# Performance work log

Hardware: AMD Instinct MI355X
Metric: run time of the kernel (lower is better)

## Reference

```python
import jax, jax.numpy as jnp
import numpy as np
from math import sqrt

D_MODEL, D_COND, N_HEADS = 512, 768, 8
B, H, W, L_COND = 8, 64, 64, 256


def setup_inputs() -> dict:
    key = jax.random.key(0)
    ks = jax.random.split(key, 7)
    return {
        "image": jax.random.normal(ks[0], (B, D_MODEL, H, W), jnp.float32),
        "cond": jax.random.normal(ks[1], (B, L_COND, D_COND), jnp.float32),
        "attention_mask": jnp.zeros((B, H * W, L_COND), jnp.float32),
        "Wq": jax.random.normal(ks[2], (D_MODEL, D_MODEL), jnp.float32) * 0.02,
        "Wk": jax.random.normal(ks[3], (D_MODEL, D_COND), jnp.float32) * 0.02,
        "Wv": jax.random.normal(ks[4], (D_MODEL, D_COND), jnp.float32) * 0.02,
        "Wo": jax.random.normal(ks[5], (D_MODEL, D_MODEL), jnp.float32) * 0.02,
        "bo": jnp.zeros((D_MODEL,), jnp.float32),
    }


def reference(image, cond, attention_mask, Wq, Wk, Wv, Wo, bo):
    b, d, h, w = image.shape
    L = h * w
    n = N_HEADS
    dh = d // n
    scale = sqrt(dh)
    # b d h w -> b l d
    x = image.reshape(b, d, L).transpose(0, 2, 1)
    # projections (torch Linear: y = x @ W.T), split heads: b l (n dh) -> b n l dh
    q = (x @ Wq.T).reshape(b, L, n, dh).transpose(0, 2, 1, 3)
    k = (cond @ Wk.T).reshape(b, -1, n, dh).transpose(0, 2, 1, 3)
    v = (cond @ Wv.T).reshape(b, -1, n, dh).transpose(0, 2, 1, 3)
    attn = jnp.einsum("bnqd,bnkd->bnqk", q, k) / scale
    attn = attn + attention_mask[:, None]  # b 1 L L_cond
    p = jax.nn.softmax(attn, axis=-1)
    o = jnp.einsum("bnqk,bnkd->bnqd", p, v)  # b n L dh
    # b n (h w) dh -> b (n dh) h w
    o = o.transpose(0, 1, 3, 2).reshape(b, d, h, w)
    # 1x1 conv == per-pixel linear over channels
    out = jnp.einsum("oc,bchw->bohw", Wo, o) + bo[None, :, None, None]
    return out
```

## Files before the change

kernel.cpp:

```cpp
#include <hip/hip_runtime.h>

typedef __bf16 bf16x8 __attribute__((ext_vector_type(8)));
typedef float f32x4 __attribute__((ext_vector_type(4)));
typedef short s4 __attribute__((ext_vector_type(4)));
typedef unsigned short ush;

#define DEV __device__ __forceinline__


DEV ush f2bf(float x){
  union { float f; unsigned u; } v; v.f = x;
  unsigned r = v.u + 0x7FFFu + ((v.u >> 16) & 1u);
  return (ush)(r >> 16);
}

DEV short bfcast(float x){
  union { __bf16 h; short s; } cv; cv.h = (__bf16)x; return cv.s;
}

DEV void gload_lds16(const ush* g, ush* l){
  __builtin_amdgcn_global_load_lds(
      (const __attribute__((address_space(1))) unsigned int*)g,
      (__attribute__((address_space(3))) unsigned int*)l, 16, 0, 0);
}

__global__ __launch_bounds__(256) void tc_kernel(const float* __restrict__ img, ush* __restrict__ xT){
  __shared__ float tile[32][34];
  const int b = blockIdx.z;
  const int l0 = blockIdx.x << 5, c0 = blockIdx.y << 5;
  const int rj = threadIdx.x >> 3, cj = threadIdx.x & 7;
  const float* src = img + ((size_t)b*512 + c0 + rj)*4096 + l0 + (cj<<2);
  float4 v = *(const float4*)src;
  *(float2*)&tile[rj][(cj<<2)]     = make_float2(v.x, v.y);
  *(float2*)&tile[rj][(cj<<2) + 2] = make_float2(v.z, v.w);
  __syncthreads();
  s4 o;
  #pragma unroll
  for (int k = 0; k < 4; ++k) o[k] = bfcast(tile[(cj<<2) + k][rj]);
  *(s4*)(xT + ((size_t)b*4096 + l0 + rj)*512 + c0 + (cj<<2)) = o;
}

__global__ __launch_bounds__(256) void cvt_kernel(const float* c0,const float* c1,const float* c2,
                                                  const float* c3,const float* c4,
                                                  ush* o0, ush* o1, ush* o2, ush* o3, ush* o4){
  const int N0=1572864, N1=262144, N2=393216, N3=393216, N4=262144;
  const int stride = gridDim.x * blockDim.x;
  for (int i = blockIdx.x*blockDim.x + threadIdx.x; i < N0+N1+N2+N3+N4; i += stride){
    int j = i; const float* s; ush* d;
    if (j < N0){ s=c0; d=o0; }
    else { j-=N0; if (j<N1){s=c1;d=o1;}
      else { j-=N1; if (j<N2){s=c2;d=o2;}
        else { j-=N2; if (j<N3){s=c3;d=o3;} else { j-=N3; s=c4; d=o4; } } } }
    d[j] = f2bf(s[j]);
  }
}

DEV void gemm_core(const ush* __restrict__ Ag, long long a_row0, int lda,
                   const ush* __restrict__ Bg, long long b_row0, int ldb,
                   int K, ush* As, ush* Bs, f32x4 acc[4][4])
{
  const int t = threadIdx.x;
  const int lane = t & 63;
  const int wid = t >> 6, wr = wid >> 1, wc = wid & 1;
  #pragma unroll
  for (int mt=0;mt<4;mt++)
    #pragma unroll
    for (int nt=0;nt<4;nt++) acc[mt][nt] = f32x4{0.f,0.f,0.f,0.f};

  const int nk = K >> 6;
  for (int kt = 0; kt < nk; ++kt){
    const int k0 = kt << 6;
    #pragma unroll
    for (int r = 0; r < 4; ++r){
      int idx = (r<<8) + t;
      int row = idx >> 3, slot = idx & 7;
      gload_lds16(Ag + (a_row0 + row)*(long long)lda + k0 + ((slot ^ (row&7))<<3), As + idx*8);
    }
    #pragma unroll
    for (int r = 0; r < 4; ++r){
      int idx = (r<<8) + t;
      int row = idx >> 3, slot = idx & 7;
      gload_lds16(Bg + (b_row0 + row)*(long long)ldb + k0 + ((slot ^ (row&7))<<3), Bs + idx*8);
    }
    __syncthreads();
    #pragma unroll
    for (int kk = 0; kk < 2; ++kk){
      bf16x8 af[4], bfv[4];
      #pragma unroll
      for (int mt=0;mt<4;mt++){
        int row = (wr<<6) + (mt<<4) + (lane & 15);
        int byte = (row<<7) + (kk<<6) + ((lane>>4)<<4);
        byte ^= (row & 7) << 4;
        af[mt] = *(const bf16x8*)((const char*)As + byte);
      }
      #pragma unroll
      for (int nt=0;nt<4;nt++){
        int row = (wc<<6) + (nt<<4) + (lane & 15);
        int byte = (row<<7) + (kk<<6) + ((lane>>4)<<4);
        byte ^= (row & 7) << 4;
        bfv[nt] = *(const bf16x8*)((const char*)Bs + byte);
      }
      #pragma unroll
      for (int mt=0;mt<4;mt++)
        #pragma unroll
        for (int nt=0;nt<4;nt++)
          acc[mt][nt] = __builtin_amdgcn_mfma_f32_16x16x32_bf16(af[mt], bfv[nt], acc[mt][nt], 0,0,0);
    }
    __syncthreads();
  }
}

__global__ __launch_bounds__(256,2) void qproj_kernel(const ush* __restrict__ xT, const ush* __restrict__ Wqb,
                                                      ush* __restrict__ Qg){
  __shared__ ush As[8192], Bs[8192];
  f32x4 acc[4][4];
  const int mb = blockIdx.x & 255, nb = blockIdx.x >> 8;
  gemm_core(xT, (long long)mb*128, 512, Wqb, (long long)nb*128, 512, 512, As, Bs, acc);
  const int lane = threadIdx.x & 63, wid = threadIdx.x >> 6, wr = wid>>1, wc = wid&1;
  #pragma unroll
  for (int mt=0;mt<4;mt++)
    #pragma unroll
    for (int nt=0;nt<4;nt++)
      #pragma unroll
      for (int r=0;r<4;r++){
        int m = mb*128 + (wr<<6) + (mt<<4) + ((lane>>4)<<2) + r;
        int n = (nb<<7) + (wc<<6) + (nt<<4) + (lane&15);
        int bb = m >> 12, l = m & 4095, hh = n >> 6, dh = n & 63;
        Qg[(((size_t)(bb*8 + hh)*4096 + l)<<6) + dh] = f2bf(acc[mt][nt][r] * 0.180336880f);
      }
}

__global__ __launch_bounds__(256,2) void kvproj_kernel(const ush* __restrict__ cb, const ush* __restrict__ Wkb,
                                                       const ush* __restrict__ Wvb, ush* __restrict__ Kg,
                                                       ush* __restrict__ Vt){
  __shared__ ush As[8192], Bs[8192];
  f32x4 acc[4][4];
  const int which = blockIdx.z;
  const int nb = blockIdx.x & 3, mb = blockIdx.x >> 2;
  gemm_core(cb, (long long)mb*128, 768, which ? Wvb : Wkb, (long long)nb*128, 768, 768, As, Bs, acc);
  const int lane = threadIdx.x & 63, wid = threadIdx.x >> 6, wr = wid>>1, wc = wid&1;
  #pragma unroll
  for (int mt=0;mt<4;mt++)
    #pragma unroll
    for (int nt=0;nt<4;nt++)
      #pragma unroll
      for (int r=0;r<4;r++){
        int m = mb*128 + (wr<<6) + (mt<<4) + ((lane>>4)<<2) + r;
        int n = (nb<<7) + (wc<<6) + (nt<<4) + (lane&15);
        int bb = m >> 8, j = m & 255;
        ush val = f2bf(acc[mt][nt][r]);
        if (!which) Kg[(((size_t)(bb*256 + j))<<9) + n] = val;
        else { int hh = n>>6, dh = n&63; Vt[(((size_t)((bb*8+hh)*64 + dh))<<8) + j] = val; }
      }
}

__global__ __launch_bounds__(512,1) void attn_kernel(const ush* __restrict__ Qg, const ush* __restrict__ Kg,
                                                     const ush* __restrict__ Vg, const float* __restrict__ mask,
                                                     ush* __restrict__ Oc){
  extern __shared__ char smem[];
  ush* Ks = (ush*)smem;
  ush* Vs = (ush*)(smem + 32768);
  const int t = threadIdx.x, lane = t & 63, wid = t >> 6;
  const int qb = blockIdx.x, h = blockIdx.y, b = blockIdx.z;
  const float L2E = 1.44269504f;

  #pragma unroll
  for (int r = 0; r < 4; ++r){
    int idx = (r<<9) + t;
    int j = idx >> 3, slot = idx & 7;
    gload_lds16(Kg + ((size_t)(b*256 + j))*512 + h*64 + ((slot ^ (j&7))<<3), Ks + idx*8);
  }
  #pragma unroll
  for (int r = 0; r < 4; ++r){
    int idx = (r<<9) + t;
    int dh = idx >> 5, slot = idx & 31;
    gload_lds16(Vg + ((size_t)((b*8 + h)*64 + dh))*256 + ((((slot&7) ^ (dh&7)) | (slot&24))<<3), Vs + idx*8);
  }
  __syncthreads();

  const int l15 = lane & 15, kg = lane >> 4;
  const ush* Qbase = Qg + ((size_t)(b*8 + h)*4096)*64;
  const int q00 = qb*1024 + wid*128;

  #pragma unroll 1
  for (int mp = 0; mp < 4; ++mp){
    const int qA = q00 + mp*32 + l15;
    const int qB = qA + 16;
    bf16x8 qf00 = *(const bf16x8*)(Qbase + (size_t)qA*64 + (kg<<3));
    bf16x8 qf01 = *(const bf16x8*)(Qbase + (size_t)qA*64 + 32 + (kg<<3));
    bf16x8 qf10 = *(const bf16x8*)(Qbase + (size_t)qB*64 + (kg<<3));
    bf16x8 qf11 = *(const bf16x8*)(Qbase + (size_t)qB*64 + 32 + (kg<<3));
    const float* mrowA = mask + ((size_t)b*4096 + qA)*256 + (kg<<2);
    const float* mrowB = mrowA + (16<<8);

    f32x4 oaccA[4], oaccB[4];
    #pragma unroll
    for (int tl=0;tl<4;++tl){ oaccA[tl] = f32x4{0.f,0.f,0.f,0.f}; oaccB[tl] = f32x4{0.f,0.f,0.f,0.f}; }
    float mA = 0.f, mB = 0.f;
    f32x4 svA = f32x4{0.f,0.f,0.f,0.f}, svB = f32x4{0.f,0.f,0.f,0.f};

    #pragma unroll 1
    for (int qt = 0; qt < 4; ++qt){
      f32x4 sA[4], sB[4];
      #pragma unroll
      for (int nt=0;nt<4;++nt){ sA[nt] = f32x4{0.f,0.f,0.f,0.f}; sB[nt] = f32x4{0.f,0.f,0.f,0.f}; }
      #pragma unroll
      for (int nt=0;nt<4;++nt){
        int row = (qt<<6) + (nt<<4) + l15;
        const char* kb = (const char*)Ks + (row<<7);
        int sw = (row&7)<<4;
        bf16x8 kf0 = *(const bf16x8*)(kb + ((kg<<4) ^ sw));
        bf16x8 kf1 = *(const bf16x8*)(kb + (((kg<<4)+64) ^ sw));
        sA[nt] = __builtin_amdgcn_mfma_f32_16x16x32_bf16(kf0, qf00, sA[nt], 0,0,0);
        sA[nt] = __builtin_amdgcn_mfma_f32_16x16x32_bf16(kf1, qf01, sA[nt], 0,0,0);
        sB[nt] = __builtin_amdgcn_mfma_f32_16x16x32_bf16(kf0, qf10, sB[nt], 0,0,0);
        sB[nt] = __builtin_amdgcn_mfma_f32_16x16x32_bf16(kf1, qf11, sB[nt], 0,0,0);
      }

      float mxA = -3.0e38f, mxB = -3.0e38f;
      #pragma unroll
      for (int nt=0;nt<4;++nt){
        float4 va = *(const float4*)(mrowA + (qt<<6) + (nt<<4));
        float4 vb = *(const float4*)(mrowB + (qt<<6) + (nt<<4));
        sA[nt][0] = fmaf(va.x, L2E, sA[nt][0]); sA[nt][1] = fmaf(va.y, L2E, sA[nt][1]);
        sA[nt][2] = fmaf(va.z, L2E, sA[nt][2]); sA[nt][3] = fmaf(va.w, L2E, sA[nt][3]);
        sB[nt][0] = fmaf(vb.x, L2E, sB[nt][0]); sB[nt][1] = fmaf(vb.y, L2E, sB[nt][1]);
        sB[nt][2] = fmaf(vb.z, L2E, sB[nt][2]); sB[nt][3] = fmaf(vb.w, L2E, sB[nt][3]);
        #pragma unroll
        for (int r=0;r<4;++r){ mxA = fmaxf(mxA, sA[nt][r]); mxB = fmaxf(mxB, sB[nt][r]); }
      }
      mxA = fmaxf(mxA, __shfl_xor(mxA, 16, 64));
      mxA = fmaxf(mxA, __shfl_xor(mxA, 32, 64));
      mxB = fmaxf(mxB, __shfl_xor(mxB, 16, 64));
      mxB = fmaxf(mxB, __shfl_xor(mxB, 32, 64));

      if (qt == 0){
        mA = mxA; mB = mxB;
      } else if (!__all(fmaxf(mxA - mA, mxB - mB) <= 8.f)){
        float mnA = fmaxf(mA, mxA), mnB = fmaxf(mB, mxB);
        float aA = exp2f(mA - mnA), aB = exp2f(mB - mnB);
        #pragma unroll
        for (int r=0;r<4;++r){ svA[r] *= aA; svB[r] *= aB; }
        #pragma unroll
        for (int tl=0;tl<4;++tl)
          #pragma unroll
          for (int r=0;r<4;++r){ oaccA[tl][r] *= aA; oaccB[tl][r] *= aB; }
        mA = mnA; mB = mnB;
      }

      #pragma unroll
      for (int nt=0;nt<4;++nt){
        s4 pA, pB;
        #pragma unroll
        for (int r=0;r<4;++r){
          float pa = exp2f(sA[nt][r] - mA);
          float pb = exp2f(sB[nt][r] - mB);
          svA[r] += pa; svB[r] += pb;
          pA[r] = bfcast(pa); pB[r] = bfcast(pb);
        }
        #pragma unroll
        for (int tl=0;tl<4;++tl){
          int dr = (tl<<4) + l15;
          int off = ((qt<<7) + (nt<<5) + (kg<<3)) ^ ((dr&7)<<4);
          s4 vf = *(const s4*)((const char*)Vs + (dr<<9) + off);
          oaccA[tl] = __builtin_amdgcn_mfma_f32_16x16x16bf16_1k(vf, pA, oaccA[tl], 0,0,0);
          oaccB[tl] = __builtin_amdgcn_mfma_f32_16x16x16bf16_1k(vf, pB, oaccB[tl], 0,0,0);
        }
      }
      __builtin_amdgcn_sched_barrier(0);
    }

    float sAt = (svA[0]+svA[1]) + (svA[2]+svA[3]);
    float sBt = (svB[0]+svB[1]) + (svB[2]+svB[3]);
    sAt += __shfl_xor(sAt, 16, 64); sAt += __shfl_xor(sAt, 32, 64);
    sBt += __shfl_xor(sBt, 16, 64); sBt += __shfl_xor(sBt, 32, 64);
    const float rlA = 1.f / sAt, rlB = 1.f / sBt;
    #pragma unroll
    for (int tl=0;tl<4;++tl){
      s4 ovA, ovB;
      #pragma unroll
      for (int r=0;r<4;++r){ ovA[r] = bfcast(oaccA[tl][r] * rlA); ovB[r] = bfcast(oaccB[tl][r] * rlB); }
      *(s4*)(Oc + (((size_t)b*4096 + qA)<<9) + h*64 + (tl<<4) + (kg<<2)) = ovA;
      *(s4*)(Oc + (((size_t)b*4096 + qB)<<9) + h*64 + (tl<<4) + (kg<<2)) = ovB;
    }
  }
}

__global__ __launch_bounds__(256,2) void oproj_kernel(const ush* __restrict__ Wob, const ush* __restrict__ Oc,
                                                      const float* __restrict__ bo, float* __restrict__ out){
  __shared__ ush As[8192], Bs[8192];
  f32x4 acc[4][4];
  const int bz = blockIdx.z;
  const int mb = blockIdx.x >> 5, nb = blockIdx.x & 31;
  gemm_core(Wob, (long long)mb*128, 512, Oc + (size_t)bz*4096*512, (long long)nb*128, 512, 512, As, Bs, acc);
  const int lane = threadIdx.x & 63, wid = threadIdx.x >> 6, wr = wid>>1, wc = wid&1;
  #pragma unroll
  for (int mt=0;mt<4;mt++)
    #pragma unroll
    for (int nt=0;nt<4;nt++){
      #pragma unroll
      for (int r=0;r<4;r++){
        int m = (mb<<7) + (wr<<6) + (mt<<4) + ((lane>>4)<<2) + r;
        int n = (nb<<7) + (wc<<6) + (nt<<4) + (lane&15);
        out[(((size_t)(bz*512 + m))<<12) + n] = acc[mt][nt][r] + bo[m];
      }
    }
}

extern "C" void kernel_launch(void* const* d_in, const int* in_sizes, int n_in,
                              void* d_out, int out_size, void* d_ws, size_t ws_size,
                              hipStream_t stream){
  const float* image = (const float*)d_in[0];
  const float* cond  = (const float*)d_in[1];
  const float* mask  = (const float*)d_in[2];
  const float* Wq    = (const float*)d_in[3];
  const float* Wk    = (const float*)d_in[4];
  const float* Wv    = (const float*)d_in[5];
  const float* Wo    = (const float*)d_in[6];
  const float* bo    = (const float*)d_in[7];
  float* out = (float*)d_out;

  char* ws = (char*)d_ws;
  ush* xT   = (ush*)(ws);
  ush* Oc   = xT;
  ush* Qg   = (ush*)(ws + 33554432);
  ush* cndb = (ush*)(ws + 67108864);
  ush* Kg   = (ush*)(ws + 70254592);
  ush* Vt   = (ush*)(ws + 72351744);
  ush* Wqb  = (ush*)(ws + 74448896);
  ush* Wkb  = (ush*)(ws + 74973184);
  ush* Wvb  = (ush*)(ws + 75759616);
  ush* Wob  = (ush*)(ws + 76546048);

  (void)hipFuncSetAttribute((const void*)attn_kernel,
                            hipFuncAttributeMaxDynamicSharedMemorySize, 65536);

  tc_kernel<<<dim3(128,16,8), 256, 0, stream>>>(image, xT);
  cvt_kernel<<<dim3(1024), 256, 0, stream>>>(cond, Wq, Wk, Wv, Wo, cndb, Wqb, Wkb, Wvb, Wob);
  qproj_kernel<<<dim3(1024), 256, 0, stream>>>(xT, Wqb, Qg);
  kvproj_kernel<<<dim3(64,1,2), 256, 0, stream>>>(cndb, Wkb, Wvb, Kg, Vt);
  attn_kernel<<<dim3(4,8,8), 512, 65536, stream>>>(Qg, Kg, Vt, mask, Oc);
  oproj_kernel<<<dim3(128,1,8), 256, 0, stream>>>(Wob, Oc, bo, out);
}
```

Measured before the change: 157.2 us.

## Fuse image transpose and bf16 conversion into Q projection GEMM

Removes the separate transpose kernel that wrote a bf16 transposed copy of the image. The Q projection now loads fp32 image tiles directly, stages them in shared memory, and transposes and converts them to bf16 into the swizzled A tile. This saves the intermediate buffer traffic and one launch. In exchange, each of the four N-blocks re-reads the fp32 image, and A-tile loading becomes synchronous with extra barriers.

```diff
diff --git a/kernel.cpp b/kernel.cpp
--- a/kernel.cpp
+++ b/kernel.cpp
@@ -2,7 +2,9 @@
 
 typedef __bf16 bf16x8 __attribute__((ext_vector_type(8)));
 typedef float f32x4 __attribute__((ext_vector_type(4)));
+typedef float f32x2 __attribute__((ext_vector_type(2)));
 typedef short s4 __attribute__((ext_vector_type(4)));
+typedef short s8v __attribute__((ext_vector_type(8)));
 typedef unsigned short ush;
 
 #define DEV __device__ __forceinline__
@@ -22,22 +24,6 @@
   __builtin_amdgcn_global_load_lds(
       (const __attribute__((address_space(1))) unsigned int*)g,
       (__attribute__((address_space(3))) unsigned int*)l, 16, 0, 0);
-}
-
-__global__ __launch_bounds__(256) void tc_kernel(const float* __restrict__ img, ush* __restrict__ xT){
-  __shared__ float tile[32][34];
-  const int b = blockIdx.z;
-  const int l0 = blockIdx.x << 5, c0 = blockIdx.y << 5;
-  const int rj = threadIdx.x >> 3, cj = threadIdx.x & 7;
-  const float* src = img + ((size_t)b*512 + c0 + rj)*4096 + l0 + (cj<<2);
-  float4 v = *(const float4*)src;
-  *(float2*)&tile[rj][(cj<<2)]     = make_float2(v.x, v.y);
-  *(float2*)&tile[rj][(cj<<2) + 2] = make_float2(v.z, v.w);
-  __syncthreads();
-  s4 o;
-  #pragma unroll
-  for (int k = 0; k < 4; ++k) o[k] = bfcast(tile[(cj<<2) + k][rj]);
-  *(s4*)(xT + ((size_t)b*4096 + l0 + rj)*512 + c0 + (cj<<2)) = o;
 }
 
 __global__ __launch_bounds__(256) void cvt_kernel(const float* c0,const float* c1,const float* c2,
@@ -110,13 +96,91 @@
   }
 }
 
-__global__ __launch_bounds__(256,2) void qproj_kernel(const ush* __restrict__ xT, const ush* __restrict__ Wqb,
+__global__ __launch_bounds__(256,2) void qproj_kernel(const float* __restrict__ img, const ush* __restrict__ Wqb,
                                                       ush* __restrict__ Qg){
+  __shared__ float stage[32*132];
   __shared__ ush As[8192], Bs[8192];
   f32x4 acc[4][4];
+  const int t = threadIdx.x;
+  const int lane = t & 63;
+  const int wid = t >> 6, wr = wid >> 1, wc = wid & 1;
   const int mb = blockIdx.x & 255, nb = blockIdx.x >> 8;
-  gemm_core(xT, (long long)mb*128, 512, Wqb, (long long)nb*128, 512, 512, As, Bs, acc);
-  const int lane = threadIdx.x & 63, wid = threadIdx.x >> 6, wr = wid>>1, wc = wid&1;
+  const int bI = mb >> 5;
+  const int l0 = (mb & 31) << 7;
+  const long long b_row0 = (long long)nb * 128;
+  const float* imb = img + ((size_t)bI * 512) * 4096 + l0;
+
+  #pragma unroll
+  for (int mt=0;mt<4;mt++)
+    #pragma unroll
+    for (int nt=0;nt<4;nt++) acc[mt][nt] = f32x4{0.f,0.f,0.f,0.f};
+
+  for (int kt = 0; kt < 8; ++kt){
+    const int k0 = kt << 6;
+    #pragma unroll
+    for (int r = 0; r < 4; ++r){
+      int idx = (r<<8) + t;
+      int row = idx >> 3, slot = idx & 7;
+      gload_lds16(Wqb + (b_row0 + row)*512LL + k0 + ((slot ^ (row&7))<<3), Bs + idx*8);
+    }
+    #pragma unroll 1
+    for (int half = 0; half < 2; ++half){
+      {
+        const int c = t >> 3, s = t & 7;
+        const float* src = imb + (size_t)(k0 + (half<<5) + c)*4096 + (s<<4);
+        float* dst = &stage[c*132 + (s<<4)];
+        #pragma unroll
+        for (int j = 0; j < 4; ++j){
+          float4 v = *(const float4*)(src + (j<<2));
+          *(float4*)(dst + (j<<2)) = v;
+        }
+      }
+      __syncthreads();
+      {
+        const int lp = t >> 2;
+        const int c8 = (t & 3) << 3;
+        f32x2 v[8];
+        #pragma unroll
+        for (int cc = 0; cc < 8; ++cc)
+          v[cc] = *(const f32x2*)&stage[(c8 + cc)*132 + (lp<<1)];
+        #pragma unroll
+        for (int r = 0; r < 2; ++r){
+          const int l = (lp<<1) + r;
+          s8v o;
+          #pragma unroll
+          for (int cc = 0; cc < 8; ++cc) o[cc] = bfcast(v[cc][r]);
+          const int slot = (half<<2) + (t & 3);
+          *(s8v*)(As + l*64 + ((slot ^ (l&7))<<3)) = o;
+        }
+      }
+      __syncthreads();
+    }
+    #pragma unroll
+    for (int kk = 0; kk < 2; ++kk){
+      bf16x8 af[4], bfv[4];
+      #pragma unroll
+      for (int mt=0;mt<4;mt++){
+        int row = (wr<<6) + (mt<<4) + (lane & 15);
+        int byte = (row<<7) + (kk<<6) + ((lane>>4)<<4);
+        byte ^= (row & 7) << 4;
+        af[mt] = *(const bf16x8*)((const char*)As + byte);
+      }
+      #pragma unroll
+      for (int nt=0;nt<4;nt++){
+        int row = (wc<<6) + (nt<<4) + (lane & 15);
+        int byte = (row<<7) + (kk<<6) + ((lane>>4)<<4);
+        byte ^= (row & 7) << 4;
+        bfv[nt] = *(const bf16x8*)((const char*)Bs + byte);
+      }
+      #pragma unroll
+      for (int mt=0;mt<4;mt++)
+        #pragma unroll
+        for (int nt=0;nt<4;nt++)
+          acc[mt][nt] = __builtin_amdgcn_mfma_f32_16x16x32_bf16(af[mt], bfv[nt], acc[mt][nt], 0,0,0);
+    }
+    __syncthreads();
+  }
+
   #pragma unroll
   for (int mt=0;mt<4;mt++)
     #pragma unroll
@@ -321,8 +385,7 @@
   float* out = (float*)d_out;
 
   char* ws = (char*)d_ws;
-  ush* xT   = (ush*)(ws);
-  ush* Oc   = xT;
+  ush* Oc   = (ush*)(ws);
   ush* Qg   = (ush*)(ws + 33554432);
   ush* cndb = (ush*)(ws + 67108864);
   ush* Kg   = (ush*)(ws + 70254592);
@@ -335,9 +398,8 @@
   (void)hipFuncSetAttribute((const void*)attn_kernel,
                             hipFuncAttributeMaxDynamicSharedMemorySize, 65536);
 
-  tc_kernel<<<dim3(128,16,8), 256, 0, stream>>>(image, xT);
   cvt_kernel<<<dim3(1024), 256, 0, stream>>>(cond, Wq, Wk, Wv, Wo, cndb, Wqb, Wkb, Wvb, Wob);
-  qproj_kernel<<<dim3(1024), 256, 0, stream>>>(xT, Wqb, Qg);
+  qproj_kernel<<<dim3(1024), 256, 0, stream>>>(image, Wqb, Qg);
   kvproj_kernel<<<dim3(64,1,2), 256, 0, stream>>>(cndb, Wkb, Wvb, Kg, Vt);
   attn_kernel<<<dim3(4,8,8), 512, 65536, stream>>>(Qg, Kg, Vt, mask, Oc);
   oproj_kernel<<<dim3(128,1,8), 256, 0, stream>>>(Wob, Oc, bo, out);
```

Result: slower. 173.2 us (+10.1%).
